# Kernel optimization log

Hardware: AMD Instinct MI355X
Metric: run time of the kernel (lower is better)

The kernel has to match this reference:

```python
import jax, jax.numpy as jnp
import numpy as np
import math

D_EMB = 1024
N_HEADS = 16
D_HEAD = D_EMB // N_HEADS
D_FF = 4 * D_EMB
BATCH = 2
SEQ = 2048
EPS = 1e-6


def setup_inputs() -> dict:
    key = jax.random.key(0)
    ks = jax.random.split(key, 12)
    s = 0.02
    return {
        "x": jax.random.normal(ks[0], (BATCH, SEQ, D_EMB), jnp.float32),
        "wq": jax.random.normal(ks[1], (D_EMB, D_EMB), jnp.float32) * s,
        "wk": jax.random.normal(ks[2], (D_EMB, D_EMB), jnp.float32) * s,
        "wv": jax.random.normal(ks[3], (D_EMB, D_EMB), jnp.float32) * s,
        "wo": jax.random.normal(ks[4], (D_EMB, D_EMB), jnp.float32) * s,
        "bo": jnp.zeros((D_EMB,), jnp.float32),
        "w1": jax.random.normal(ks[5], (D_FF, D_EMB), jnp.float32) * s,
        "b1": jnp.zeros((D_FF,), jnp.float32),
        "w2": jax.random.normal(ks[6], (D_EMB, D_FF), jnp.float32) * s,
        "b2": jnp.zeros((D_EMB,), jnp.float32),
        "ln1_s": jnp.ones((D_EMB,), jnp.float32),
        "ln1_b": jnp.zeros((D_EMB,), jnp.float32),
        "ln2_s": jnp.ones((D_EMB,), jnp.float32),
        "ln2_b": jnp.zeros((D_EMB,), jnp.float32),
    }


def _layernorm(x, scale, shift):
    mean = jnp.mean(x, axis=-1, keepdims=True)
    var = jnp.mean(jnp.square(x - mean), axis=-1, keepdims=True)  # unbiased=False
    return scale * (x - mean) / jnp.sqrt(var + EPS) + shift


def _gelu_tanh(x):
    c = math.sqrt(2.0 / math.pi)
    return 0.5 * x * (1.0 + jnp.tanh(c * (x + 0.044715 * x * x * x)))


def _attention(x, wq, wk, wv, wo, bo):
    B, S, _ = x.shape
    q = (x @ wq.T).reshape(B, S, N_HEADS, D_HEAD).transpose(0, 2, 1, 3)
    k = (x @ wk.T).reshape(B, S, N_HEADS, D_HEAD).transpose(0, 2, 1, 3)
    v = (x @ wv.T).reshape(B, S, N_HEADS, D_HEAD).transpose(0, 2, 1, 3)
    scores = jnp.einsum("bhqd,bhkd->bhqk", q, k)
    causal = jnp.triu(jnp.ones((S, S), bool), k=1)
    scores = jnp.where(causal, -jnp.inf, scores)
    weights = jax.nn.softmax(scores / math.sqrt(D_HEAD), axis=-1)
    ctx = jnp.einsum("bhqk,bhkd->bhqd", weights, v)
    ctx = ctx.transpose(0, 2, 1, 3).reshape(B, S, D_EMB)
    return ctx @ wo.T + bo


def reference(x, wq, wk, wv, wo, bo, w1, b1, w2, b2, ln1_s, ln1_b, ln2_s, ln2_b):
    # pre-norm attention block (dropout in eval mode = identity)
    h = x + _attention(_layernorm(x, ln1_s, ln1_b), wq, wk, wv, wo, bo)
    # pre-norm MLP with tanh-approx GeLU
    y = _layernorm(h, ln2_s, ln2_b)
    y = _gelu_tanh(y @ w1.T + b1) @ w2.T + b2
    return h + y
```

## Files before the change

### kernel.cpp

```cpp
#include <hip/hip_runtime.h>
#include <math.h>

typedef unsigned short u16;
typedef __attribute__((ext_vector_type(8))) __bf16 bf16x8v;
typedef __attribute__((ext_vector_type(8))) unsigned short ushort8v;
typedef __attribute__((ext_vector_type(4))) unsigned short ushort4v;
typedef __attribute__((ext_vector_type(4))) float f32x4v;

#define D_EMBD 1024
#define NHEADS 16
#define DHEAD  64
#define DFF    4096
#define BATCHN 2
#define SEQL   2048
#define TOK    (BATCHN*SEQL)

#define EPI_BF16_GELU    2
#define EPI_BF16_QKV     3
#define EPI_BF16_PART    5

__device__ __forceinline__ float bf2f(u16 s) {
  return __builtin_bit_cast(float, (unsigned)s << 16);
}
__device__ __forceinline__ u16 f2bf(float f) {
  unsigned u = __builtin_bit_cast(unsigned, f);
  unsigned r = u + 0x7fffu + ((u >> 16) & 1u);
  return (u16)(r >> 16);
}
__device__ __forceinline__ u16 f2bf_trunc(float f) {
  return (u16)(__builtin_bit_cast(unsigned, f) >> 16);
}

#define GLOAD16(gp, lp)                                                        \
  __builtin_amdgcn_global_load_lds(                                            \
      (__attribute__((address_space(1))) void*)(void*)(gp),                    \
      (__attribute__((address_space(3))) void*)(void*)(lp), 16, 0, 0)

__global__ __launch_bounds__(256) void cvt_all_kernel(const float* __restrict__ wq,
                                                      const float* __restrict__ wk,
                                                      const float* __restrict__ wv,
                                                      const float* __restrict__ wo,
                                                      const float* __restrict__ w1,
                                                      const float* __restrict__ w2,
                                                      u16* __restrict__ wcat,
                                                      u16* __restrict__ wob,
                                                      u16* __restrict__ w1b,
                                                      u16* __restrict__ w2b) {
  int bid = blockIdx.x;
  const float* src;
  u16* dst;
  int loc;
  if (bid < 4096) {
    int seg = bid >> 10;
    loc = (bid & 1023) * 256 + threadIdx.x;
    src = (seg == 0) ? wq : (seg == 1) ? wk : (seg == 2) ? wv : wo;
    dst = (seg == 0) ? wcat : (seg == 1) ? wcat + 1048576
                            : (seg == 2) ? wcat + 2097152 : wob;
  } else if (bid < 8192) {
    loc = (bid - 4096) * 256 + threadIdx.x;
    src = w1; dst = w1b;
  } else {
    loc = (bid - 8192) * 256 + threadIdx.x;
    src = w2; dst = w2b;
  }
  float4 v = ((const float4*)src)[loc];
  ushort4 o;
  o.x = f2bf(v.x); o.y = f2bf(v.y); o.z = f2bf(v.z); o.w = f2bf(v.w);
  ((ushort4*)dst)[loc] = o;
}

__global__ __launch_bounds__(256) void ln_kernel(const float* __restrict__ x,
                                                 const float* __restrict__ sc,
                                                 const float* __restrict__ sh,
                                                 u16* __restrict__ out) {
  int row = blockIdx.x, tid = threadIdx.x;
  const float4* xr = (const float4*)(x + (size_t)row * D_EMBD);
  float4 v = xr[tid];
  float s  = (v.x + v.y) + (v.z + v.w);
  float s2 = (v.x * v.x + v.y * v.y) + (v.z * v.z + v.w * v.w);
#pragma unroll
  for (int off = 32; off; off >>= 1) {
    s  += __shfl_xor(s, off, 64);
    s2 += __shfl_xor(s2, off, 64);
  }
  __shared__ float rs[4], rs2[4];
  int wave = tid >> 6, lane = tid & 63;
  if (lane == 0) { rs[wave] = s; rs2[wave] = s2; }
  __syncthreads();
  s  = (rs[0] + rs[1]) + (rs[2] + rs[3]);
  s2 = (rs2[0] + rs2[1]) + (rs2[2] + rs2[3]);
  float mean = s * (1.f / 1024.f);
  float var  = s2 * (1.f / 1024.f) - mean * mean;
  float rstd = rsqrtf(var + 1e-6f);
  float4 scv = ((const float4*)sc)[tid];
  float4 shv = ((const float4*)sh)[tid];
  ushort4 o;
  o.x = f2bf((v.x - mean) * rstd * scv.x + shv.x);
  o.y = f2bf((v.y - mean) * rstd * scv.y + shv.y);
  o.z = f2bf((v.z - mean) * rstd * scv.z + shv.z);
  o.w = f2bf((v.w - mean) * rstd * scv.w + shv.w);
  ((ushort4*)(out + (size_t)row * D_EMBD))[tid] = o;
}

__global__ __launch_bounds__(256) void ln2f_kernel(const u16* __restrict__ parts,
                                                   const float* __restrict__ x,
                                                   const float* __restrict__ bo,
                                                   const float* __restrict__ sc,
                                                   const float* __restrict__ sh,
                                                   float* __restrict__ hbuf,
                                                   u16* __restrict__ ybuf) {
  int row = blockIdx.x, tid = threadIdx.x;
  size_t base4 = (size_t)row * 256 + tid;
  float4 v = ((const float4*)x)[base4];
  float4 bv = ((const float4*)bo)[tid];
  v.x += bv.x; v.y += bv.y; v.z += bv.z; v.w += bv.w;
#pragma unroll
  for (int p = 0; p < 4; ++p) {
    ushort4 u = ((const ushort4*)parts)[(size_t)p * 1048576 + base4];
    v.x += bf2f(u.x); v.y += bf2f(u.y); v.z += bf2f(u.z); v.w += bf2f(u.w);
  }
  ((float4*)hbuf)[base4] = v;
  float s  = (v.x + v.y) + (v.z + v.w);
  float s2 = (v.x * v.x + v.y * v.y) + (v.z * v.z + v.w * v.w);
#pragma unroll
  for (int off = 32; off; off >>= 1) {
    s  += __shfl_xor(s, off, 64);
    s2 += __shfl_xor(s2, off, 64);
  }
  __shared__ float rs[4], rs2[4];
  int wave = tid >> 6, lane = tid & 63;
  if (lane == 0) { rs[wave] = s; rs2[wave] = s2; }
  __syncthreads();
  s  = (rs[0] + rs[1]) + (rs[2] + rs[3]);
  s2 = (rs2[0] + rs2[1]) + (rs2[2] + rs2[3]);
  float mean = s * (1.f / 1024.f);
  float var  = s2 * (1.f / 1024.f) - mean * mean;
  float rstd = rsqrtf(var + 1e-6f);
  float4 scv = ((const float4*)sc)[tid];
  float4 shv = ((const float4*)sh)[tid];
  ushort4 o;
  o.x = f2bf((v.x - mean) * rstd * scv.x + shv.x);
  o.y = f2bf((v.y - mean) * rstd * scv.y + shv.y);
  o.z = f2bf((v.z - mean) * rstd * scv.z + shv.z);
  o.w = f2bf((v.w - mean) * rstd * scv.w + shv.w);
  ((ushort4*)ybuf)[base4] = o;
}

__global__ __launch_bounds__(256) void reduce_w2_kernel(const u16* __restrict__ parts,
                                                        const float* __restrict__ resid,
                                                        const float* __restrict__ bias,
                                                        float* __restrict__ out) {
  int i = blockIdx.x * 256 + threadIdx.x;
  float4 r = ((const float4*)resid)[i];
  float4 bi = ((const float4*)bias)[i & 255];
  float s0 = 0, s1 = 0, s2 = 0, s3 = 0;
#pragma unroll
  for (int p = 0; p < 4; ++p) {
    ushort4 u = ((const ushort4*)parts)[(size_t)p * 1048576 + i];
    s0 += bf2f(u.x); s1 += bf2f(u.y); s2 += bf2f(u.z); s3 += bf2f(u.w);
  }
  float4 o = {s0 + r.x + bi.x, s1 + r.y + bi.y, s2 + r.z + bi.z, s3 + r.w + bi.w};
  ((float4*)out)[i] = o;
}

#define GBAR  __builtin_amdgcn_s_barrier()
#define LGKM0 do { asm volatile("s_waitcnt lgkmcnt(0)" ::: "memory"); \
                   __builtin_amdgcn_sched_barrier(0); } while (0)

template <int EPI>
__global__ __launch_bounds__(512, 2) void gemm256(const u16* __restrict__ A,
                                                  const u16* __restrict__ W,
                                                  u16* __restrict__ Cb,
                                                  const float* __restrict__ bias,
                                                  int M, int N, int K) {
  __shared__ __align__(16) u16 sm[65536];
  const int tid = threadIdx.x;
  const int wave = tid >> 6, lane = tid & 63;
  const int lr = lane & 15, quad = lane >> 4;
  const int wm = wave >> 2, wn = wave & 3;
  const int gx = gridDim.x, gy = gridDim.y;
  const int nwg = gx * gy * gridDim.z;
  const int bid = blockIdx.x + gx * (blockIdx.y + gy * blockIdx.z);
  const int swz = (bid & 7) * (nwg >> 3) + (bid >> 3);
  const int bx = swz % gx;
  const int r1 = swz / gx;
  const int by = r1 % gy, bz = r1 / gy;
  const int m0 = by * 256, n0 = bx * 256;
  const int KC = K / gridDim.z;
  const int kbeg = bz * KC;
  const int NT = KC >> 6;
  const size_t poff = (size_t)bz * ((size_t)M * N);

  const int r8 = lane >> 3;
  const int sslot = (lane & 7) ^ r8;
  const int rb0 = wave * 2;
  const int sx = lr & 7;

  auto stA = [&](int bb, int h, int tk) {
#pragma unroll
    for (int s = 0; s < 2; ++s) {
      const u16* gp = A + (size_t)(m0 + h * 128 + (rb0 + s) * 8 + r8) * K +
                      (kbeg + tk * 64 + sslot * 8);
      GLOAD16(gp, (char*)sm + bb * 65536 + h * 16384 + (rb0 + s) * 1024);
    }
  };
  auto stB = [&](int bb, int h, int tk) {
#pragma unroll
    for (int s = 0; s < 2; ++s) {
      const u16* gp = W + (size_t)(n0 + h * 128 + (rb0 + s) * 8 + r8) * K +
                      (kbeg + tk * 64 + sslot * 8);
      GLOAD16(gp, (char*)sm + bb * 65536 + 32768 + h * 16384 + (rb0 + s) * 1024);
    }
  };
  auto ldA = [&](bf16x8v (&av)[4][2], int mh, int cur) {
#pragma unroll
    for (int j2 = 0; j2 < 4; ++j2) {
      int row = (2 * (mh * 4 + j2) + wm) * 16 + lr;
#pragma unroll
      for (int kk = 0; kk < 2; ++kk) {
        int slot = (kk * 4 + quad) ^ sx;
        av[j2][kk] = *(const bf16x8v*)(sm + cur * 32768 + row * 64 + slot * 8);
      }
    }
  };
  auto ldB = [&](bf16x8v (&bv)[2][2], int nh, int cur) {
#pragma unroll
    for (int i2 = 0; i2 < 2; ++i2) {
      int row = (wn + 4 * (nh * 2 + i2)) * 16 + lr;
#pragma unroll
      for (int kk = 0; kk < 2; ++kk) {
        int slot = (kk * 4 + quad) ^ sx;
        bv[i2][kk] = *(const bf16x8v*)(sm + cur * 32768 + 16384 + row * 64 + slot * 8);
      }
    }
  };

  f32x4v acc[8][4];
#pragma unroll
  for (int j = 0; j < 8; ++j)
#pragma unroll
    for (int i = 0; i < 4; ++i) {
      f32x4v z = {0.f, 0.f, 0.f, 0.f};
      acc[j][i] = z;
    }
  bf16x8v av[4][2], bv0[2][2], bv1[2][2];

  auto MMA = [&](int mh, int nh, bf16x8v (&a)[4][2], bf16x8v (&b)[2][2]) {
    GBAR;
    LGKM0;
    __builtin_amdgcn_s_setprio(1);
#pragma unroll
    for (int j2 = 0; j2 < 4; ++j2)
#pragma unroll
      for (int i2 = 0; i2 < 2; ++i2)
#pragma unroll
        for (int kk = 0; kk < 2; ++kk)
          acc[mh * 4 + j2][nh * 2 + i2] = __builtin_amdgcn_mfma_f32_16x16x32_bf16(
              a[j2][kk], b[i2][kk], acc[mh * 4 + j2][nh * 2 + i2], 0, 0, 0);
    __builtin_amdgcn_s_setprio(0);
    __builtin_amdgcn_sched_barrier(0);
    GBAR;
  };

  stA(0, 0, 0); stB(0, 0, 0); stA(0, 1, 0); stB(0, 1, 0);
  stA(1, 0, 1); stB(1, 1, 1);
  asm volatile("s_waitcnt vmcnt(4)" ::: "memory");
  GBAR;

  for (int t = 0; t < NT; ++t) {
    const int cur = t & 1, nb = cur ^ 1;
    const bool p1 = (t + 1 < NT), p2 = (t + 2 < NT);
    ldA(av, 0, cur); ldB(bv0, 0, cur);
    if (p1) stB(nb, 0, t + 1);
    MMA(0, 0, av, bv0);
    ldB(bv1, 1, cur);
    if (p1) stA(nb, 1, t + 1);
    MMA(0, 1, av, bv1);
    ldA(av, 1, cur);
    if (p2) stA(cur, 0, t + 2);
    MMA(1, 1, av, bv1);
    if (p2) stB(cur, 1, t + 2);
    if (p2) { asm volatile("s_waitcnt vmcnt(4)" ::: "memory"); }
    else    { asm volatile("s_waitcnt vmcnt(0)" ::: "memory"); }
    MMA(1, 0, av, bv0);
  }

  const bool qsc = (EPI == EPI_BF16_QKV) && (n0 < 1024);
#pragma unroll
  for (int j = 0; j < 8; ++j) {
    int gr = m0 + (2 * j + wm) * 16 + quad * 4;
#pragma unroll
    for (int i = 0; i < 4; ++i) {
      int gc = n0 + (wn + 4 * i) * 16 + lr;
      float bi = 0.f;
      if constexpr (EPI == EPI_BF16_GELU) bi = bias[gc];
#pragma unroll
      for (int r = 0; r < 4; ++r) {
        size_t idx = (size_t)(gr + r) * N + gc;
        float v = acc[j][i][r];
        if constexpr (EPI == EPI_BF16_PART) {
          Cb[poff + idx] = f2bf(v);
        } else if constexpr (EPI == EPI_BF16_QKV) {
          Cb[idx] = f2bf(qsc ? v * 0.125f : v);
        } else {
          v += bi;
          float z = 0.7978845608028654f * (v + 0.044715f * v * v * v);
          float tt = 2.f / (1.f + __expf(-2.f * z)) - 1.f;
          Cb[idx] = f2bf(0.5f * v * (1.f + tt));
        }
      }
    }
  }
}

#define VTS 72
__device__ __forceinline__ void stage_k8(const u16* Kbase, int ks, u16* kfbuf,
                                         int wave, int lr, int quad) {
  int key = ((wave >> 1) << 4) + lr;
  int c8 = ((wave & 1) << 2) + quad;
  GLOAD16(Kbase + (size_t)(ks + key) * 3072 + c8 * 8, (char*)kfbuf + wave * 1024);
}
__device__ __forceinline__ void load_v(const u16* Vbase, int ks, int vkey0, int vc8,
                                       ushort8v& va, ushort8v& vb) {
  va = *(const ushort8v*)(Vbase + (size_t)(ks + vkey0) * 3072 + vc8 * 8);
  vb = *(const ushort8v*)(Vbase + (size_t)(ks + vkey0 + 1) * 3072 + vc8 * 8);
}
__device__ __forceinline__ void write_vt(u16* vt, int vc8, int vcol,
                                         ushort8v va, ushort8v vb) {
#pragma unroll
  for (int j = 0; j < 8; ++j) {
    unsigned pk = (unsigned)va[j] | ((unsigned)vb[j] << 16);
    *(unsigned*)(vt + (size_t)(vc8 * 8 + j) * VTS + vcol) = pk;
  }
}

__global__ __launch_bounds__(512) void attn_kernel(const u16* __restrict__ qkv,
                                                   u16* __restrict__ ctx) {
  __shared__ u16 Kf[2][4096];
  __shared__ u16 Vt[2][64 * VTS];
  int tid = threadIdx.x;
  int wave = tid >> 6, lane = tid & 63;
  int lr = lane & 15, quad = lane >> 4;
  int id = blockIdx.x;
  int bh = id & 31;
  int t = 15 - (id >> 5);
  int b = bh >> 4, h = bh & 15;
  int q0 = t * 128;
  const u16* qkvb = qkv + (size_t)(b * SEQL) * 3072;
  int qrow = q0 + wave * 16 + lr;
  const u16* Qp = qkvb + (size_t)qrow * 3072 + h * 64 + quad * 8;
  bf16x8v qf0 = *(const bf16x8v*)(Qp);
  bf16x8v qf1 = *(const bf16x8v*)(Qp + 32);
  const u16* Kbase = qkvb + 1024 + h * 64;
  const u16* Vbase = qkvb + 2048 + h * 64;
  const bool vstager = (tid < 256);
  int vkey0 = ((tid & 255) >> 3) * 2, vc8 = tid & 7;
  int vcol = vkey0 ^ (vc8 << 2);

  float m = -INFINITY, l = 0.f;
  f32x4v accO[4];
#pragma unroll
  for (int r = 0; r < 4; r++) {
    f32x4v z = {0.f, 0.f, 0.f, 0.f};
    accO[r] = z;
  }

  int nkt = 2 * t + 2;
  {
    stage_k8(Kbase, 0, Kf[0], wave, lr, quad);
    if (vstager) {
      ushort8v va, vb;
      load_v(Vbase, 0, vkey0, vc8, va, vb);
      write_vt(Vt[0], vc8, vcol, va, vb);
    }
  }
  __syncthreads();

  for (int kt = 0; kt < nkt; ++kt) {
    int cur = kt & 1, nxt = cur ^ 1;
    ushort8v va, vb;
    bool pre = (kt + 1 < nkt);
    if (pre) {
      stage_k8(Kbase, (kt + 1) * 64, Kf[nxt], wave, lr, quad);
      if (vstager) load_v(Vbase, (kt + 1) * 64, vkey0, vc8, va, vb);
    }
    bool active = !(kt == 2 * t + 1 && wave < 4);
    if (active) {
      const bf16x8v* Kc = (const bf16x8v*)Kf[cur];
      const u16* Vc = Vt[cur];
      f32x4v accS[4];
#pragma unroll
      for (int jb = 0; jb < 4; jb++) {
        f32x4v z = {0.f, 0.f, 0.f, 0.f};
        accS[jb] = z;
      }
#pragma unroll
      for (int jb = 0; jb < 4; jb++) {
        accS[jb] = __builtin_amdgcn_mfma_f32_16x16x32_bf16(Kc[((jb * 2 + 0) << 6) + lane], qf0, accS[jb], 0, 0, 0);
        accS[jb] = __builtin_amdgcn_mfma_f32_16x16x32_bf16(Kc[((jb * 2 + 1) << 6) + lane], qf1, accS[jb], 0, 0, 0);
      }
      if (kt >= 2 * t) {
        int kb = (kt - 2 * t) << 6;
#pragma unroll
        for (int jb = 0; jb < 4; jb++)
#pragma unroll
          for (int r = 0; r < 4; r++)
            if (kb + jb * 16 + quad * 4 + r > wave * 16 + lr) accS[jb][r] = -INFINITY;
      }
      float smax = accS[0][0];
#pragma unroll
      for (int jb = 0; jb < 4; jb++)
#pragma unroll
        for (int r = 0; r < 4; r++) smax = fmaxf(smax, accS[jb][r]);
      smax = fmaxf(smax, __shfl_xor(smax, 16, 64));
      smax = fmaxf(smax, __shfl_xor(smax, 32, 64));
      float mn = fmaxf(m, smax);
      float alpha = __expf(m - mn);
      m = mn;
      float ps = 0.f;
#pragma unroll
      for (int jb = 0; jb < 4; jb++)
#pragma unroll
        for (int r = 0; r < 4; r++) {
          accS[jb][r] = __expf(accS[jb][r] - mn);
          ps += accS[jb][r];
        }
      ps += __shfl_xor(ps, 16, 64);
      ps += __shfl_xor(ps, 32, 64);
      l = l * alpha + ps;
      float ar[4];
#pragma unroll
      for (int r = 0; r < 4; r++) ar[r] = __shfl(alpha, quad * 4 + r, 16);
#pragma unroll
      for (int nb = 0; nb < 4; nb++)
#pragma unroll
        for (int r = 0; r < 4; r++) accO[nb][r] *= ar[r];
#pragma unroll
      for (int kk = 0; kk < 2; ++kk) {
        ushort8v pp;
#pragma unroll
        for (int j = 0; j < 4; ++j) {
          pp[j]     = f2bf_trunc(accS[2 * kk][j]);
          pp[j + 4] = f2bf_trunc(accS[2 * kk + 1][j]);
        }
        bf16x8v pav = __builtin_bit_cast(bf16x8v, pp);
#pragma unroll
        for (int nb = 0; nb < 4; nb++) {
          int dim = nb * 16 + lr;
          int f = (nb * 2 + (lr >> 3)) & 7;
          int col1 = (kk * 32 + quad * 4) ^ (f << 2);
          ushort4v v0 = *(const ushort4v*)(Vc + dim * VTS + col1);
          ushort4v v1 = *(const ushort4v*)(Vc + dim * VTS + (col1 ^ 16));
          ushort8v vv;
#pragma unroll
          for (int j = 0; j < 4; ++j) { vv[j] = v0[j]; vv[j + 4] = v1[j]; }
          accO[nb] = __builtin_amdgcn_mfma_f32_16x16x32_bf16(pav, __builtin_bit_cast(bf16x8v, vv), accO[nb], 0, 0, 0);
        }
      }
    }
    if (pre && vstager) write_vt(Vt[nxt], vc8, vcol, va, vb);
    __syncthreads();
  }
  float linv = 1.f / l;
  float rr[4];
#pragma unroll
  for (int r = 0; r < 4; r++) rr[r] = __shfl(linv, quad * 4 + r, 16);
#pragma unroll
  for (int nb = 0; nb < 4; nb++)
#pragma unroll
    for (int r = 0; r < 4; r++) {
      int rowg = q0 + wave * 16 + quad * 4 + r;
      ctx[(size_t)(b * SEQL + rowg) * D_EMBD + h * 64 + nb * 16 + lr] =
          f2bf(accO[nb][r] * rr[r]);
    }
}

extern "C" void kernel_launch(void* const* d_in, const int* in_sizes, int n_in,
                              void* d_out, int out_size, void* d_ws, size_t ws_size,
                              hipStream_t stream) {
  const float* x    = (const float*)d_in[0];
  const float* wq   = (const float*)d_in[1];
  const float* wk   = (const float*)d_in[2];
  const float* wv   = (const float*)d_in[3];
  const float* wo   = (const float*)d_in[4];
  const float* bo   = (const float*)d_in[5];
  const float* w1   = (const float*)d_in[6];
  const float* b1   = (const float*)d_in[7];
  const float* w2   = (const float*)d_in[8];
  const float* b2   = (const float*)d_in[9];
  const float* ln1s = (const float*)d_in[10];
  const float* ln1b = (const float*)d_in[11];
  const float* ln2s = (const float*)d_in[12];
  const float* ln2b = (const float*)d_in[13];
  float* out = (float*)d_out;

  char* base = (char*)d_ws;
  size_t off = 0;
  auto alloc = [&](size_t bytes) {
    char* r = base + off;
    off += (bytes + 255) & ~(size_t)255;
    return r;
  };
  u16*   wcat = (u16*)alloc((size_t)3072 * 1024 * 2);
  u16*   wob  = (u16*)alloc((size_t)1024 * 1024 * 2);
  u16*   w1b  = (u16*)alloc((size_t)4096 * 1024 * 2);
  u16*   w2b  = (u16*)alloc((size_t)1024 * 4096 * 2);
  u16*   xn   = (u16*)alloc((size_t)TOK * 1024 * 2);
  u16*   qkv  = (u16*)alloc((size_t)TOK * 3072 * 2);
  u16*   ctx  = (u16*)alloc((size_t)TOK * 1024 * 2);
  float* hbuf = (float*)alloc((size_t)TOK * 1024 * 4);
  u16*   ybuf = (u16*)alloc((size_t)TOK * 1024 * 2);
  u16*   gbuf = (u16*)alloc((size_t)TOK * 4096 * 2);
  u16* woP = (u16*)xn;
  u16* w2P = (u16*)xn;

  cvt_all_kernel<<<12288, 256, 0, stream>>>(wq, wk, wv, wo, w1, w2,
                                            wcat, wob, w1b, w2b);
  ln_kernel<<<TOK, 256, 0, stream>>>(x, ln1s, ln1b, xn);
  gemm256<EPI_BF16_QKV><<<dim3(12, 16), 512, 0, stream>>>(
      xn, wcat, qkv, nullptr, TOK, 3072, 1024);
  attn_kernel<<<512, 512, 0, stream>>>(qkv, ctx);
  gemm256<EPI_BF16_PART><<<dim3(4, 16, 4), 512, 0, stream>>>(
      ctx, wob, woP, nullptr, TOK, 1024, 1024);
  ln2f_kernel<<<TOK, 256, 0, stream>>>(woP, x, bo, ln2s, ln2b, hbuf, ybuf);
  gemm256<EPI_BF16_GELU><<<dim3(16, 16), 512, 0, stream>>>(
      ybuf, w1b, gbuf, b1, TOK, 4096, 1024);
  gemm256<EPI_BF16_PART><<<dim3(4, 16, 4), 512, 0, stream>>>(
      gbuf, w2b, w2P, nullptr, TOK, 1024, 4096);
  reduce_w2_kernel<<<4096, 256, 0, stream>>>(w2P, hbuf, b2, out);
}
```

Baseline: 334.6 us.

## Merge weight-cast and LN1 kernels, merge GEMM MMA phases, shrink attention tiles

Folds the weight conversion and the first layernorm into one launch so a kernel boundary disappears. In the GEMM, the four half-tile MMA phases become two larger phases, with the B loads and the global stages grouped together. Attention now uses 64-query blocks of 256 threads (1024 blocks) instead of 128-query blocks of 512 threads, which drops the idle-wave masking on the diagonal tile and gives more blocks for load balance. In exchange, K/V tiles are reloaded twice as often per query row, and the GEMM's load/compute interleave changes, so more bf16x8 fragments (av, bv0, bv1) are held live at once, which may raise register pressure.

```diff
diff --git a/kernel.cpp b/kernel.cpp
--- a/kernel.cpp
+++ b/kernel.cpp
@@ -36,44 +36,45 @@
       (__attribute__((address_space(1))) void*)(void*)(gp),                    \
       (__attribute__((address_space(3))) void*)(void*)(lp), 16, 0, 0)
 
-__global__ __launch_bounds__(256) void cvt_all_kernel(const float* __restrict__ wq,
-                                                      const float* __restrict__ wk,
-                                                      const float* __restrict__ wv,
-                                                      const float* __restrict__ wo,
-                                                      const float* __restrict__ w1,
-                                                      const float* __restrict__ w2,
-                                                      u16* __restrict__ wcat,
-                                                      u16* __restrict__ wob,
-                                                      u16* __restrict__ w1b,
-                                                      u16* __restrict__ w2b) {
-  int bid = blockIdx.x;
-  const float* src;
-  u16* dst;
-  int loc;
-  if (bid < 4096) {
-    int seg = bid >> 10;
-    loc = (bid & 1023) * 256 + threadIdx.x;
-    src = (seg == 0) ? wq : (seg == 1) ? wk : (seg == 2) ? wv : wo;
-    dst = (seg == 0) ? wcat : (seg == 1) ? wcat + 1048576
-                            : (seg == 2) ? wcat + 2097152 : wob;
-  } else if (bid < 8192) {
-    loc = (bid - 4096) * 256 + threadIdx.x;
-    src = w1; dst = w1b;
-  } else {
-    loc = (bid - 8192) * 256 + threadIdx.x;
-    src = w2; dst = w2b;
-  }
-  float4 v = ((const float4*)src)[loc];
-  ushort4 o;
-  o.x = f2bf(v.x); o.y = f2bf(v.y); o.z = f2bf(v.z); o.w = f2bf(v.w);
-  ((ushort4*)dst)[loc] = o;
-}
-
-__global__ __launch_bounds__(256) void ln_kernel(const float* __restrict__ x,
-                                                 const float* __restrict__ sc,
-                                                 const float* __restrict__ sh,
-                                                 u16* __restrict__ out) {
-  int row = blockIdx.x, tid = threadIdx.x;
+__global__ __launch_bounds__(256) void prep_kernel(const float* __restrict__ wq,
+                                                   const float* __restrict__ wk,
+                                                   const float* __restrict__ wv,
+                                                   const float* __restrict__ wo,
+                                                   const float* __restrict__ w1,
+                                                   const float* __restrict__ w2,
+                                                   u16* __restrict__ wcat,
+                                                   u16* __restrict__ wob,
+                                                   u16* __restrict__ w1b,
+                                                   u16* __restrict__ w2b,
+                                                   const float* __restrict__ x,
+                                                   const float* __restrict__ sc,
+                                                   const float* __restrict__ sh,
+                                                   u16* __restrict__ xn) {
+  int bid = blockIdx.x, tid = threadIdx.x;
+  if (bid < 12288) {
+    const float* src;
+    u16* dst;
+    int loc;
+    if (bid < 4096) {
+      int seg = bid >> 10;
+      loc = (bid & 1023) * 256 + tid;
+      src = (seg == 0) ? wq : (seg == 1) ? wk : (seg == 2) ? wv : wo;
+      dst = (seg == 0) ? wcat : (seg == 1) ? wcat + 1048576
+                              : (seg == 2) ? wcat + 2097152 : wob;
+    } else if (bid < 8192) {
+      loc = (bid - 4096) * 256 + tid;
+      src = w1; dst = w1b;
+    } else {
+      loc = (bid - 8192) * 256 + tid;
+      src = w2; dst = w2b;
+    }
+    float4 v = ((const float4*)src)[loc];
+    ushort4 o;
+    o.x = f2bf(v.x); o.y = f2bf(v.y); o.z = f2bf(v.z); o.w = f2bf(v.w);
+    ((ushort4*)dst)[loc] = o;
+    return;
+  }
+  int row = bid - 12288;
   const float4* xr = (const float4*)(x + (size_t)row * D_EMBD);
   float4 v = xr[tid];
   float s  = (v.x + v.y) + (v.z + v.w);
@@ -99,7 +100,7 @@
   o.y = f2bf((v.y - mean) * rstd * scv.y + shv.y);
   o.z = f2bf((v.z - mean) * rstd * scv.z + shv.z);
   o.w = f2bf((v.w - mean) * rstd * scv.w + shv.w);
-  ((ushort4*)(out + (size_t)row * D_EMBD))[tid] = o;
+  ((ushort4*)(xn + (size_t)row * D_EMBD))[tid] = o;
 }
 
 __global__ __launch_bounds__(256) void ln2f_kernel(const u16* __restrict__ parts,
@@ -245,7 +246,7 @@
     }
   bf16x8v av[4][2], bv0[2][2], bv1[2][2];
 
-  auto MMA = [&](int mh, int nh, bf16x8v (&a)[4][2], bf16x8v (&b)[2][2]) {
+  auto MMA32 = [&](int mh) {
     GBAR;
     LGKM0;
     __builtin_amdgcn_s_setprio(1);
@@ -254,9 +255,12 @@
 #pragma unroll
       for (int i2 = 0; i2 < 2; ++i2)
 #pragma unroll
-        for (int kk = 0; kk < 2; ++kk)
-          acc[mh * 4 + j2][nh * 2 + i2] = __builtin_amdgcn_mfma_f32_16x16x32_bf16(
-              a[j2][kk], b[i2][kk], acc[mh * 4 + j2][nh * 2 + i2], 0, 0, 0);
+        for (int kk = 0; kk < 2; ++kk) {
+          acc[mh * 4 + j2][i2] = __builtin_amdgcn_mfma_f32_16x16x32_bf16(
+              av[j2][kk], bv0[i2][kk], acc[mh * 4 + j2][i2], 0, 0, 0);
+          acc[mh * 4 + j2][2 + i2] = __builtin_amdgcn_mfma_f32_16x16x32_bf16(
+              av[j2][kk], bv1[i2][kk], acc[mh * 4 + j2][2 + i2], 0, 0, 0);
+        }
     __builtin_amdgcn_s_setprio(0);
     __builtin_amdgcn_sched_barrier(0);
     GBAR;
@@ -270,19 +274,14 @@
   for (int t = 0; t < NT; ++t) {
     const int cur = t & 1, nb = cur ^ 1;
     const bool p1 = (t + 1 < NT), p2 = (t + 2 < NT);
-    ldA(av, 0, cur); ldB(bv0, 0, cur);
-    if (p1) stB(nb, 0, t + 1);
-    MMA(0, 0, av, bv0);
-    ldB(bv1, 1, cur);
-    if (p1) stA(nb, 1, t + 1);
-    MMA(0, 1, av, bv1);
+    ldA(av, 0, cur); ldB(bv0, 0, cur); ldB(bv1, 1, cur);
+    if (p1) { stB(nb, 0, t + 1); stA(nb, 1, t + 1); }
+    MMA32(0);
     ldA(av, 1, cur);
-    if (p2) stA(cur, 0, t + 2);
-    MMA(1, 1, av, bv1);
-    if (p2) stB(cur, 1, t + 2);
+    if (p2) { stA(cur, 0, t + 2); stB(cur, 1, t + 2); }
     if (p2) { asm volatile("s_waitcnt vmcnt(4)" ::: "memory"); }
     else    { asm volatile("s_waitcnt vmcnt(0)" ::: "memory"); }
-    MMA(1, 0, av, bv0);
+    MMA32(1);
   }
 
   const bool qsc = (EPI == EPI_BF16_QKV) && (n0 < 1024);
@@ -314,11 +313,15 @@
 }
 
 #define VTS 72
-__device__ __forceinline__ void stage_k8(const u16* Kbase, int ks, u16* kfbuf,
-                                         int wave, int lr, int quad) {
-  int key = ((wave >> 1) << 4) + lr;
-  int c8 = ((wave & 1) << 2) + quad;
-  GLOAD16(Kbase + (size_t)(ks + key) * 3072 + c8 * 8, (char*)kfbuf + wave * 1024);
+__device__ __forceinline__ void stage_k(const u16* Kbase, int ks, u16* kfbuf,
+                                        int wave, int lr, int quad) {
+#pragma unroll
+  for (int p = 0; p < 2; ++p) {
+    int q = wave * 2 + p;
+    int key = ((q >> 1) << 4) + lr;
+    int c8 = ((q & 1) << 2) + quad;
+    GLOAD16(Kbase + (size_t)(ks + key) * 3072 + c8 * 8, (char*)kfbuf + q * 1024);
+  }
 }
 __device__ __forceinline__ void load_v(const u16* Vbase, int ks, int vkey0, int vc8,
                                        ushort8v& va, ushort8v& vb) {
@@ -334,7 +337,7 @@
   }
 }
 
-__global__ __launch_bounds__(512) void attn_kernel(const u16* __restrict__ qkv,
+__global__ __launch_bounds__(256) void attn_kernel(const u16* __restrict__ qkv,
                                                    u16* __restrict__ ctx) {
   __shared__ u16 Kf[2][4096];
   __shared__ u16 Vt[2][64 * VTS];
@@ -343,9 +346,9 @@
   int lr = lane & 15, quad = lane >> 4;
   int id = blockIdx.x;
   int bh = id & 31;
-  int t = 15 - (id >> 5);
+  int t = 31 - (id >> 5);
   int b = bh >> 4, h = bh & 15;
-  int q0 = t * 128;
+  int q0 = t * 64;
   const u16* qkvb = qkv + (size_t)(b * SEQL) * 3072;
   int qrow = q0 + wave * 16 + lr;
   const u16* Qp = qkvb + (size_t)qrow * 3072 + h * 64 + quad * 8;
@@ -353,8 +356,7 @@
   bf16x8v qf1 = *(const bf16x8v*)(Qp + 32);
   const u16* Kbase = qkvb + 1024 + h * 64;
   const u16* Vbase = qkvb + 2048 + h * 64;
-  const bool vstager = (tid < 256);
-  int vkey0 = ((tid & 255) >> 3) * 2, vc8 = tid & 7;
+  int vkey0 = (tid >> 3) * 2, vc8 = tid & 7;
   int vcol = vkey0 ^ (vc8 << 2);
 
   float m = -INFINITY, l = 0.f;
@@ -365,14 +367,12 @@
     accO[r] = z;
   }
 
-  int nkt = 2 * t + 2;
+  int nkt = t + 1;
   {
-    stage_k8(Kbase, 0, Kf[0], wave, lr, quad);
-    if (vstager) {
-      ushort8v va, vb;
-      load_v(Vbase, 0, vkey0, vc8, va, vb);
-      write_vt(Vt[0], vc8, vcol, va, vb);
-    }
+    stage_k(Kbase, 0, Kf[0], wave, lr, quad);
+    ushort8v va, vb;
+    load_v(Vbase, 0, vkey0, vc8, va, vb);
+    write_vt(Vt[0], vc8, vcol, va, vb);
   }
   __syncthreads();
 
@@ -381,84 +381,80 @@
     ushort8v va, vb;
     bool pre = (kt + 1 < nkt);
     if (pre) {
-      stage_k8(Kbase, (kt + 1) * 64, Kf[nxt], wave, lr, quad);
-      if (vstager) load_v(Vbase, (kt + 1) * 64, vkey0, vc8, va, vb);
-    }
-    bool active = !(kt == 2 * t + 1 && wave < 4);
-    if (active) {
-      const bf16x8v* Kc = (const bf16x8v*)Kf[cur];
-      const u16* Vc = Vt[cur];
-      f32x4v accS[4];
-#pragma unroll
-      for (int jb = 0; jb < 4; jb++) {
-        f32x4v z = {0.f, 0.f, 0.f, 0.f};
-        accS[jb] = z;
+      stage_k(Kbase, (kt + 1) * 64, Kf[nxt], wave, lr, quad);
+      load_v(Vbase, (kt + 1) * 64, vkey0, vc8, va, vb);
+    }
+    const bf16x8v* Kc = (const bf16x8v*)Kf[cur];
+    const u16* Vc = Vt[cur];
+    f32x4v accS[4];
+#pragma unroll
+    for (int jb = 0; jb < 4; jb++) {
+      f32x4v z = {0.f, 0.f, 0.f, 0.f};
+      accS[jb] = z;
+    }
+#pragma unroll
+    for (int jb = 0; jb < 4; jb++) {
+      accS[jb] = __builtin_amdgcn_mfma_f32_16x16x32_bf16(Kc[((jb * 2 + 0) << 6) + lane], qf0, accS[jb], 0, 0, 0);
+      accS[jb] = __builtin_amdgcn_mfma_f32_16x16x32_bf16(Kc[((jb * 2 + 1) << 6) + lane], qf1, accS[jb], 0, 0, 0);
+    }
+    if (kt == t) {
+#pragma unroll
+      for (int jb = 0; jb < 4; jb++)
+#pragma unroll
+        for (int r = 0; r < 4; r++)
+          if (jb * 16 + quad * 4 + r > wave * 16 + lr) accS[jb][r] = -INFINITY;
+    }
+    float smax = accS[0][0];
+#pragma unroll
+    for (int jb = 0; jb < 4; jb++)
+#pragma unroll
+      for (int r = 0; r < 4; r++) smax = fmaxf(smax, accS[jb][r]);
+    smax = fmaxf(smax, __shfl_xor(smax, 16, 64));
+    smax = fmaxf(smax, __shfl_xor(smax, 32, 64));
+    float mn = fmaxf(m, smax);
+    float alpha = __expf(m - mn);
+    m = mn;
+    float ps = 0.f;
+#pragma unroll
+    for (int jb = 0; jb < 4; jb++)
+#pragma unroll
+      for (int r = 0; r < 4; r++) {
+        accS[jb][r] = __expf(accS[jb][r] - mn);
+        ps += accS[jb][r];
       }
-#pragma unroll
-      for (int jb = 0; jb < 4; jb++) {
-        accS[jb] = __builtin_amdgcn_mfma_f32_16x16x32_bf16(Kc[((jb * 2 + 0) << 6) + lane], qf0, accS[jb], 0, 0, 0);
-        accS[jb] = __builtin_amdgcn_mfma_f32_16x16x32_bf16(Kc[((jb * 2 + 1) << 6) + lane], qf1, accS[jb], 0, 0, 0);
+    ps += __shfl_xor(ps, 16, 64);
+    ps += __shfl_xor(ps, 32, 64);
+    l = l * alpha + ps;
+    float ar[4];
+#pragma unroll
+    for (int r = 0; r < 4; r++) ar[r] = __shfl(alpha, quad * 4 + r, 16);
+#pragma unroll
+    for (int nb = 0; nb < 4; nb++)
+#pragma unroll
+      for (int r = 0; r < 4; r++) accO[nb][r] *= ar[r];
+#pragma unroll
+    for (int kk = 0; kk < 2; ++kk) {
+      ushort8v pp;
+#pragma unroll
+      for (int j = 0; j < 4; ++j) {
+        pp[j]     = f2bf_trunc(accS[2 * kk][j]);
+        pp[j + 4] = f2bf_trunc(accS[2 * kk + 1][j]);
       }
-      if (kt >= 2 * t) {
-        int kb = (kt - 2 * t) << 6;
-#pragma unroll
-        for (int jb = 0; jb < 4; jb++)
-#pragma unroll
-          for (int r = 0; r < 4; r++)
-            if (kb + jb * 16 + quad * 4 + r > wave * 16 + lr) accS[jb][r] = -INFINITY;
+      bf16x8v pav = __builtin_bit_cast(bf16x8v, pp);
+#pragma unroll
+      for (int nb = 0; nb < 4; nb++) {
+        int dim = nb * 16 + lr;
+        int f = (nb * 2 + (lr >> 3)) & 7;
+        int col1 = (kk * 32 + quad * 4) ^ (f << 2);
+        ushort4v v0 = *(const ushort4v*)(Vc + dim * VTS + col1);
+        ushort4v v1 = *(const ushort4v*)(Vc + dim * VTS + (col1 ^ 16));
+        ushort8v vv;
+#pragma unroll
+        for (int j = 0; j < 4; ++j) { vv[j] = v0[j]; vv[j + 4] = v1[j]; }
+        accO[nb] = __builtin_amdgcn_mfma_f32_16x16x32_bf16(pav, __builtin_bit_cast(bf16x8v, vv), accO[nb], 0, 0, 0);
       }
-      float smax = accS[0][0];
-#pragma unroll
-      for (int jb = 0; jb < 4; jb++)
-#pragma unroll
-        for (int r = 0; r < 4; r++) smax = fmaxf(smax, accS[jb][r]);
-      smax = fmaxf(smax, __shfl_xor(smax, 16, 64));
-      smax = fmaxf(smax, __shfl_xor(smax, 32, 64));
-      float mn = fmaxf(m, smax);
-      float alpha = __expf(m - mn);
-      m = mn;
-      float ps = 0.f;
-#pragma unroll
-      for (int jb = 0; jb < 4; jb++)
-#pragma unroll
-        for (int r = 0; r < 4; r++) {
-          accS[jb][r] = __expf(accS[jb][r] - mn);
-          ps += accS[jb][r];
-        }
-      ps += __shfl_xor(ps, 16, 64);
-      ps += __shfl_xor(ps, 32, 64);
-      l = l * alpha + ps;
-      float ar[4];
-#pragma unroll
-      for (int r = 0; r < 4; r++) ar[r] = __shfl(alpha, quad * 4 + r, 16);
-#pragma unroll
-      for (int nb = 0; nb < 4; nb++)
-#pragma unroll
-        for (int r = 0; r < 4; r++) accO[nb][r] *= ar[r];
-#pragma unroll
-      for (int kk = 0; kk < 2; ++kk) {
-        ushort8v pp;
-#pragma unroll
-        for (int j = 0; j < 4; ++j) {
-          pp[j]     = f2bf_trunc(accS[2 * kk][j]);
-          pp[j + 4] = f2bf_trunc(accS[2 * kk + 1][j]);
-        }
-        bf16x8v pav = __builtin_bit_cast(bf16x8v, pp);
-#pragma unroll
-        for (int nb = 0; nb < 4; nb++) {
-          int dim = nb * 16 + lr;
-          int f = (nb * 2 + (lr >> 3)) & 7;
-          int col1 = (kk * 32 + quad * 4) ^ (f << 2);
-          ushort4v v0 = *(const ushort4v*)(Vc + dim * VTS + col1);
-          ushort4v v1 = *(const ushort4v*)(Vc + dim * VTS + (col1 ^ 16));
-          ushort8v vv;
-#pragma unroll
-          for (int j = 0; j < 4; ++j) { vv[j] = v0[j]; vv[j + 4] = v1[j]; }
-          accO[nb] = __builtin_amdgcn_mfma_f32_16x16x32_bf16(pav, __builtin_bit_cast(bf16x8v, vv), accO[nb], 0, 0, 0);
-        }
-      }
-    }
-    if (pre && vstager) write_vt(Vt[nxt], vc8, vcol, va, vb);
+    }
+    if (pre) write_vt(Vt[nxt], vc8, vcol, va, vb);
     __syncthreads();
   }
   float linv = 1.f / l;
@@ -514,12 +510,12 @@
   u16* woP = (u16*)xn;
   u16* w2P = (u16*)xn;
 
-  cvt_all_kernel<<<12288, 256, 0, stream>>>(wq, wk, wv, wo, w1, w2,
-                                            wcat, wob, w1b, w2b);
-  ln_kernel<<<TOK, 256, 0, stream>>>(x, ln1s, ln1b, xn);
+  prep_kernel<<<16384, 256, 0, stream>>>(wq, wk, wv, wo, w1, w2,
+                                         wcat, wob, w1b, w2b,
+                                         x, ln1s, ln1b, xn);
   gemm256<EPI_BF16_QKV><<<dim3(12, 16), 512, 0, stream>>>(
       xn, wcat, qkv, nullptr, TOK, 3072, 1024);
-  attn_kernel<<<512, 512, 0, stream>>>(qkv, ctx);
+  attn_kernel<<<1024, 256, 0, stream>>>(qkv, ctx);
   gemm256<EPI_BF16_PART><<<dim3(4, 16, 4), 512, 0, stream>>>(
       ctx, wob, woP, nullptr, TOK, 1024, 1024);
   ln2f_kernel<<<TOK, 256, 0, stream>>>(woP, x, bo, ln2s, ln2b, hbuf, ybuf);
```

After: 326.5 us. 2.4% less time.
